# Kernel optimization log

Hardware: AMD Instinct MI355X
Metric: run time of the kernel (lower is better)

## Reference

```python
import jax, jax.numpy as jnp
import numpy as np

B, T, I, H, L, O = 2048, 512, 1, 64, 2, 1


def _lstm_layer(x, Wih, Whh, b):
    """Single LSTM layer, batch_first x: [B, T, in] -> [B, T, H].
    PyTorch gate order: i, f, g, o. b = b_ih + b_hh (folded)."""
    Bn = x.shape[0]
    Hn = Whh.shape[1]
    # Precompute input contribution for all timesteps (hoisted out of scan)
    xg = jnp.einsum('bti,gi->btg', x, Wih) + b  # [B, T, 4H]

    def step(carry, xg_t):
        h, c = carry
        g = xg_t + h @ Whh.T  # [B, 4H]
        i, f, gg, o = jnp.split(g, 4, axis=-1)
        i = jax.nn.sigmoid(i)
        f = jax.nn.sigmoid(f)
        gg = jnp.tanh(gg)
        o = jax.nn.sigmoid(o)
        c = f * c + i * gg
        h = o * jnp.tanh(c)
        return (h, c), h

    h0 = jnp.zeros((Bn, Hn), x.dtype)
    c0 = jnp.zeros((Bn, Hn), x.dtype)
    (_, _), hs = jax.lax.scan(step, (h0, c0), jnp.swapaxes(xg, 0, 1))  # hs: [T, B, H]
    return jnp.swapaxes(hs, 0, 1)


def setup_inputs() -> dict:
    key = jax.random.key(0)
    ks = jax.random.split(key, 11)
    s = 1.0 / np.sqrt(H)  # torch default uniform bound
    u = lambda k, shp: jax.random.uniform(k, shp, jnp.float32, -s, s)
    return {
        'x': jax.random.normal(ks[0], (B, T, I), jnp.float32),
        'Wih0': u(ks[1], (4 * H, I)),
        'Whh0': u(ks[2], (4 * H, H)),
        'bih0': u(ks[3], (4 * H,)),
        'bhh0': u(ks[4], (4 * H,)),
        'Wih1': u(ks[5], (4 * H, H)),
        'Whh1': u(ks[6], (4 * H, H)),
        'bih1': u(ks[7], (4 * H,)),
        'bhh1': u(ks[8], (4 * H,)),
        'fcW': u(ks[9], (O, H)),
        'fcb': u(ks[10], (O,)),
    }


def reference(x, Wih0, Whh0, bih0, bhh0, Wih1, Whh1, bih1, bhh1, fcW, fcb):
    h1 = _lstm_layer(x, Wih0, Whh0, bih0 + bhh0)   # [B, T, H]
    h2 = _lstm_layer(h1, Wih1, Whh1, bih1 + bhh1)  # [B, T, H]
    return h2[:, -1, :] @ fcW.T + fcb               # [B, O]
```

## Files before the change

### kernel.cpp

```cpp
#include <hip/hip_runtime.h>


#define TT 512
#define HH 64
#define BT 8

typedef __attribute__((ext_vector_type(8))) short short8;
typedef __attribute__((ext_vector_type(4))) float f32x4;

#define MFMA16 __builtin_amdgcn_mfma_f32_16x16x32_bf16

__device__ __forceinline__ float sigm(float x) {
    return __builtin_amdgcn_rcpf(1.f + __expf(-x));
}
__device__ __forceinline__ float tanh_f(float x) {
    return 1.f - 2.f * __builtin_amdgcn_rcpf(1.f + __expf(2.f * x));
}
__device__ __forceinline__ void cvt8(const float* p, short8& hi, short8& lo) {
    #pragma unroll
    for (int i = 0; i < 8; ++i) {
        float v = p[i];
        unsigned short h = (unsigned short)(__float_as_uint(v) >> 16);
        float r = v - __uint_as_float(((unsigned)h) << 16);
        unsigned short l = (unsigned short)(__float_as_uint(r) >> 16);
        hi[i] = (short)h;
        lo[i] = (short)l;
    }
}
__device__ __forceinline__ void split1(float v, unsigned short& h, unsigned short& l) {
    h = (unsigned short)(__float_as_uint(v) >> 16);
    float r = v - __uint_as_float(((unsigned)h) << 16);
    l = (unsigned short)(__float_as_uint(r) >> 16);
}
__device__ __forceinline__ float gate4(float pi, float pf, float pg, float po, float& c) {
    float gi = sigm(pi), gf = sigm(pf), gg = tanh_f(pg), go = sigm(po);
    c = fmaf(gf, c, gi * gg);
    return go * tanh_f(c);
}
__device__ __forceinline__ float dpp_ror8(float v) {
    return __int_as_float(__builtin_amdgcn_update_dpp(
        0, __float_as_int(v), 0x128, 0xF, 0xF, true));
}

__global__ __launch_bounds__(1024) void lstm_mfma(
    const float* __restrict__ x,
    const float* __restrict__ Wih0, const float* __restrict__ Whh0,
    const float* __restrict__ bih0, const float* __restrict__ bhh0,
    const float* __restrict__ Wih1, const float* __restrict__ Whh1,
    const float* __restrict__ bih1, const float* __restrict__ bhh1,
    const float* __restrict__ fcW, const float* __restrict__ fcb,
    float* __restrict__ out)
{
    __shared__ float xs[BT][TT + 1];
    __shared__ __align__(16) short aH1[2][2][2][64][8];
    __shared__ __align__(16) short aH2[2][2][2][64][8];
    __shared__ float hF[BT][HH + 1];
    __shared__ float fcw_s[HH];

    const int t    = threadIdx.x;
    const int lane = t & 63;
    const int w    = t >> 6;
    const bool isL1 = (w < 8);
    const int wv   = w & 7;
    const int b0   = blockIdx.x * BT;
    const int m    = lane & 15;
    const int q    = lane >> 4;

    for (int i = t; i < BT * TT; i += 1024)
        xs[i >> 9][i & (TT - 1)] = x[(size_t)(b0 + (i >> 9)) * TT + (i & (TT - 1))];
    {
        int* z1 = (int*)aH1;
        for (int i = t; i < 2048; i += 1024) z1[i] = 0;
        int* z2 = (int*)aH2;
        for (int i = t; i < 2048; i += 1024) z2[i] = 0;
    }
    if (t < HH) fcw_s[t] = fcW[t];

    short8 aWh[2][4], aWl[2][4];
    {
        const float* Ws01 = isL1 ? Whh0 : Wih1;
        #pragma unroll
        for (int i = 0; i < 2; ++i) {
            const int mtg = 2 * wv + i;
            const int rho = (m & 3) * 64 + 4 * mtg + (m >> 2);
            cvt8(Ws01 + rho * HH +      q * 8, aWh[i][0], aWl[i][0]);
            cvt8(Ws01 + rho * HH + 32 + q * 8, aWh[i][1], aWl[i][1]);
            if (!isL1) {
                cvt8(Whh1 + rho * HH +      q * 8, aWh[i][2], aWl[i][2]);
                cvt8(Whh1 + rho * HH + 32 + q * 8, aWh[i][3], aWl[i][3]);
            }
        }
    }

    const int ts  = (m >> 3) & 1;
    const int jpk = 8 * wv + 4 * ts + q;
    const int bpk = m & 7;
    float wxb[4], bia[4];
    #pragma unroll
    for (int v = 0; v < 4; ++v) {
        if (isL1) {
            wxb[v] = Wih0[v * 64 + jpk];
            bia[v] = bih0[v * 64 + jpk] + bhh0[v * 64 + jpk];
        } else {
            wxb[v] = 0.f;
            bia[v] = bih1[v * 64 + jpk] + bhh1[v * 64 + jpk];
        }
    }
    const int skt = jpk >> 5;
    const int ssl = bpk + 16 * ((jpk >> 3) & 3);
    const int sse = jpk & 7;
    float c = 0.f;

    __syncthreads();

    #pragma unroll 2
    for (int k = 0; k < TT; ++k) {
        const int p = k & 1, pn = p ^ 1;

        if (isL1) {
            short8 bh0 = *(const short8*)&aH1[p][0][0][lane][0];
            short8 bl0 = *(const short8*)&aH1[p][0][1][lane][0];
            short8 bh1 = *(const short8*)&aH1[p][1][0][lane][0];
            short8 bl1 = *(const short8*)&aH1[p][1][1][lane][0];
            f32x4 acc0 = {0.f, 0.f, 0.f, 0.f}, acc1 = acc0;
            acc0 = MFMA16(aWh[0][0], bh0, acc0, 0, 0, 0);
            acc0 = MFMA16(aWl[0][0], bh0, acc0, 0, 0, 0);
            acc0 = MFMA16(aWh[0][0], bl0, acc0, 0, 0, 0);
            acc0 = MFMA16(aWh[0][1], bh1, acc0, 0, 0, 0);
            acc0 = MFMA16(aWl[0][1], bh1, acc0, 0, 0, 0);
            acc0 = MFMA16(aWh[0][1], bl1, acc0, 0, 0, 0);
            acc1 = MFMA16(aWh[1][0], bh0, acc1, 0, 0, 0);
            acc1 = MFMA16(aWl[1][0], bh0, acc1, 0, 0, 0);
            acc1 = MFMA16(aWh[1][0], bl0, acc1, 0, 0, 0);
            acc1 = MFMA16(aWh[1][1], bh1, acc1, 0, 0, 0);
            acc1 = MFMA16(aWl[1][1], bh1, acc1, 0, 0, 0);
            acc1 = MFMA16(aWh[1][1], bl1, acc1, 0, 0, 0);
            f32x4 mv, pk;
            #pragma unroll
            for (int r = 0; r < 4; ++r) mv[r] = dpp_ror8(acc1[r]);
            #pragma unroll
            for (int r = 0; r < 4; ++r) pk[r] = (m < 8) ? acc0[r] : mv[r];
            float xb = xs[bpk][k];
            float h1 = gate4(pk[0] + fmaf(wxb[0], xb, bia[0]),
                             pk[1] + fmaf(wxb[1], xb, bia[1]),
                             pk[2] + fmaf(wxb[2], xb, bia[2]),
                             pk[3] + fmaf(wxb[3], xb, bia[3]), c);
            unsigned short hh, hl;
            split1(h1, hh, hl);
            aH1[pn][skt][0][ssl][sse] = (short)hh;
            aH1[pn][skt][1][ssl][sse] = (short)hl;
        } else if (k > 0) {
            short8 b1h0 = *(const short8*)&aH1[p][0][0][lane][0];
            short8 b1l0 = *(const short8*)&aH1[p][0][1][lane][0];
            short8 b1h1 = *(const short8*)&aH1[p][1][0][lane][0];
            short8 b1l1 = *(const short8*)&aH1[p][1][1][lane][0];
            short8 b2h0 = *(const short8*)&aH2[p][0][0][lane][0];
            short8 b2l0 = *(const short8*)&aH2[p][0][1][lane][0];
            short8 b2h1 = *(const short8*)&aH2[p][1][0][lane][0];
            short8 b2l1 = *(const short8*)&aH2[p][1][1][lane][0];
            f32x4 acc0 = {0.f, 0.f, 0.f, 0.f}, acc1 = acc0;
            acc0 = MFMA16(aWh[0][0], b1h0, acc0, 0, 0, 0);
            acc0 = MFMA16(aWl[0][0], b1h0, acc0, 0, 0, 0);
            acc0 = MFMA16(aWh[0][0], b1l0, acc0, 0, 0, 0);
            acc0 = MFMA16(aWh[0][1], b1h1, acc0, 0, 0, 0);
            acc0 = MFMA16(aWl[0][1], b1h1, acc0, 0, 0, 0);
            acc0 = MFMA16(aWh[0][1], b1l1, acc0, 0, 0, 0);
            acc0 = MFMA16(aWh[0][2], b2h0, acc0, 0, 0, 0);
            acc0 = MFMA16(aWl[0][2], b2h0, acc0, 0, 0, 0);
            acc0 = MFMA16(aWh[0][2], b2l0, acc0, 0, 0, 0);
            acc0 = MFMA16(aWh[0][3], b2h1, acc0, 0, 0, 0);
            acc0 = MFMA16(aWl[0][3], b2h1, acc0, 0, 0, 0);
            acc0 = MFMA16(aWh[0][3], b2l1, acc0, 0, 0, 0);
            acc1 = MFMA16(aWh[1][0], b1h0, acc1, 0, 0, 0);
            acc1 = MFMA16(aWl[1][0], b1h0, acc1, 0, 0, 0);
            acc1 = MFMA16(aWh[1][0], b1l0, acc1, 0, 0, 0);
            acc1 = MFMA16(aWh[1][1], b1h1, acc1, 0, 0, 0);
            acc1 = MFMA16(aWl[1][1], b1h1, acc1, 0, 0, 0);
            acc1 = MFMA16(aWh[1][1], b1l1, acc1, 0, 0, 0);
            acc1 = MFMA16(aWh[1][2], b2h0, acc1, 0, 0, 0);
            acc1 = MFMA16(aWl[1][2], b2h0, acc1, 0, 0, 0);
            acc1 = MFMA16(aWh[1][2], b2l0, acc1, 0, 0, 0);
            acc1 = MFMA16(aWh[1][3], b2h1, acc1, 0, 0, 0);
            acc1 = MFMA16(aWl[1][3], b2h1, acc1, 0, 0, 0);
            acc1 = MFMA16(aWh[1][3], b2l1, acc1, 0, 0, 0);
            f32x4 mv, pk;
            #pragma unroll
            for (int r = 0; r < 4; ++r) mv[r] = dpp_ror8(acc1[r]);
            #pragma unroll
            for (int r = 0; r < 4; ++r) pk[r] = (m < 8) ? acc0[r] : mv[r];
            float h2 = gate4(pk[0] + bia[0], pk[1] + bia[1],
                             pk[2] + bia[2], pk[3] + bia[3], c);
            unsigned short hh, hl;
            split1(h2, hh, hl);
            aH2[pn][skt][0][ssl][sse] = (short)hh;
            aH2[pn][skt][1][ssl][sse] = (short)hl;
        }
        __syncthreads();
    }

    if (!isL1) {
        short8 b1h0 = *(const short8*)&aH1[0][0][0][lane][0];
        short8 b1l0 = *(const short8*)&aH1[0][0][1][lane][0];
        short8 b1h1 = *(const short8*)&aH1[0][1][0][lane][0];
        short8 b1l1 = *(const short8*)&aH1[0][1][1][lane][0];
        short8 b2h0 = *(const short8*)&aH2[0][0][0][lane][0];
        short8 b2l0 = *(const short8*)&aH2[0][0][1][lane][0];
        short8 b2h1 = *(const short8*)&aH2[0][1][0][lane][0];
        short8 b2l1 = *(const short8*)&aH2[0][1][1][lane][0];
        f32x4 acc0 = {0.f, 0.f, 0.f, 0.f}, acc1 = acc0;
        acc0 = MFMA16(aWh[0][0], b1h0, acc0, 0, 0, 0);
        acc0 = MFMA16(aWl[0][0], b1h0, acc0, 0, 0, 0);
        acc0 = MFMA16(aWh[0][0], b1l0, acc0, 0, 0, 0);
        acc0 = MFMA16(aWh[0][1], b1h1, acc0, 0, 0, 0);
        acc0 = MFMA16(aWl[0][1], b1h1, acc0, 0, 0, 0);
        acc0 = MFMA16(aWh[0][1], b1l1, acc0, 0, 0, 0);
        acc0 = MFMA16(aWh[0][2], b2h0, acc0, 0, 0, 0);
        acc0 = MFMA16(aWl[0][2], b2h0, acc0, 0, 0, 0);
        acc0 = MFMA16(aWh[0][2], b2l0, acc0, 0, 0, 0);
        acc0 = MFMA16(aWh[0][3], b2h1, acc0, 0, 0, 0);
        acc0 = MFMA16(aWl[0][3], b2h1, acc0, 0, 0, 0);
        acc0 = MFMA16(aWh[0][3], b2l1, acc0, 0, 0, 0);
        acc1 = MFMA16(aWh[1][0], b1h0, acc1, 0, 0, 0);
        acc1 = MFMA16(aWl[1][0], b1h0, acc1, 0, 0, 0);
        acc1 = MFMA16(aWh[1][0], b1l0, acc1, 0, 0, 0);
        acc1 = MFMA16(aWh[1][1], b1h1, acc1, 0, 0, 0);
        acc1 = MFMA16(aWl[1][1], b1h1, acc1, 0, 0, 0);
        acc1 = MFMA16(aWh[1][1], b1l1, acc1, 0, 0, 0);
        acc1 = MFMA16(aWh[1][2], b2h0, acc1, 0, 0, 0);
        acc1 = MFMA16(aWl[1][2], b2h0, acc1, 0, 0, 0);
        acc1 = MFMA16(aWh[1][2], b2l0, acc1, 0, 0, 0);
        acc1 = MFMA16(aWh[1][3], b2h1, acc1, 0, 0, 0);
        acc1 = MFMA16(aWl[1][3], b2h1, acc1, 0, 0, 0);
        acc1 = MFMA16(aWh[1][3], b2l1, acc1, 0, 0, 0);
        f32x4 mv, pk;
        #pragma unroll
        for (int r = 0; r < 4; ++r) mv[r] = dpp_ror8(acc1[r]);
        #pragma unroll
        for (int r = 0; r < 4; ++r) pk[r] = (m < 8) ? acc0[r] : mv[r];
        float h2 = gate4(pk[0] + bia[0], pk[1] + bia[1],
                         pk[2] + bia[2], pk[3] + bia[3], c);
        hF[bpk][jpk] = h2;
    }
    __syncthreads();

    if (t < BT) {
        float s = fcb[0];
        #pragma unroll 8
        for (int j = 0; j < HH; ++j)
            s = fmaf(hF[t][j], fcw_s[j], s);
        out[b0 + t] = s;
    }
}

extern "C" void kernel_launch(void* const* d_in, const int* in_sizes, int n_in,
                              void* d_out, int out_size, void* d_ws, size_t ws_size,
                              hipStream_t stream) {
    const float* x    = (const float*)d_in[0];
    const float* Wih0 = (const float*)d_in[1];
    const float* Whh0 = (const float*)d_in[2];
    const float* bih0 = (const float*)d_in[3];
    const float* bhh0 = (const float*)d_in[4];
    const float* Wih1 = (const float*)d_in[5];
    const float* Whh1 = (const float*)d_in[6];
    const float* bih1 = (const float*)d_in[7];
    const float* bhh1 = (const float*)d_in[8];
    const float* fcW  = (const float*)d_in[9];
    const float* fcb  = (const float*)d_in[10];
    float* out = (float*)d_out;

    lstm_mfma<<<dim3(2048 / BT), dim3(1024), 0, stream>>>(
        x, Wih0, Whh0, bih0, bhh0, Wih1, Whh1, bih1, bhh1, fcW, fcb, out);
}
```

Measured before the change: 492.4 us.

## Replace split-bf16 MFMA with split-int8 fixed-point MFMA and unify layer waves

Switches the recurrent matmuls from three-term split-bf16 MFMA to a two-level int8 fixed-point split (hi/lo bytes) using the i32 16x16x64 int8 MFMA, scaling weights and hidden states to fixed-point. It also restructures the work split so every wave handles both layers: one lane half computes layer 1 and the other half layer 2. This cuts the MFMA count per step from 12/24 to 9 per wave and halves LDS traffic for h. In exchange it adds quantization error from dropping the lo*lo term and fixed-point rounding, plus conversion overhead per step.

```diff
diff --git a/kernel.cpp b/kernel.cpp
--- a/kernel.cpp
+++ b/kernel.cpp
@@ -5,32 +5,19 @@
 #define HH 64
 #define BT 8
 
-typedef __attribute__((ext_vector_type(8))) short short8;
-typedef __attribute__((ext_vector_type(4))) float f32x4;
+typedef __attribute__((ext_vector_type(4))) int i32x4;
 
-#define MFMA16 __builtin_amdgcn_mfma_f32_16x16x32_bf16
+#define MFMAI8 __builtin_amdgcn_mfma_i32_16x16x64_i8
+
+#define WSCALE 260096.0f
+#define HSCALE 32512.0f
+constexpr float C_MID = (float)(256.0 / (260096.0 * 32512.0));
 
 __device__ __forceinline__ float sigm(float x) {
     return __builtin_amdgcn_rcpf(1.f + __expf(-x));
 }
 __device__ __forceinline__ float tanh_f(float x) {
     return 1.f - 2.f * __builtin_amdgcn_rcpf(1.f + __expf(2.f * x));
-}
-__device__ __forceinline__ void cvt8(const float* p, short8& hi, short8& lo) {
-    #pragma unroll
-    for (int i = 0; i < 8; ++i) {
-        float v = p[i];
-        unsigned short h = (unsigned short)(__float_as_uint(v) >> 16);
-        float r = v - __uint_as_float(((unsigned)h) << 16);
-        unsigned short l = (unsigned short)(__float_as_uint(r) >> 16);
-        hi[i] = (short)h;
-        lo[i] = (short)l;
-    }
-}
-__device__ __forceinline__ void split1(float v, unsigned short& h, unsigned short& l) {
-    h = (unsigned short)(__float_as_uint(v) >> 16);
-    float r = v - __uint_as_float(((unsigned)h) << 16);
-    l = (unsigned short)(__float_as_uint(r) >> 16);
 }
 __device__ __forceinline__ float gate4(float pi, float pf, float pg, float po, float& c) {
     float gi = sigm(pi), gf = sigm(pf), gg = tanh_f(pg), go = sigm(po);
@@ -40,6 +27,21 @@
 __device__ __forceinline__ float dpp_ror8(float v) {
     return __int_as_float(__builtin_amdgcn_update_dpp(
         0, __float_as_int(v), 0x128, 0xF, 0xF, true));
+}
+__device__ __forceinline__ void cvtW16(const float* __restrict__ p, i32x4& hi, i32x4& lo) {
+    #pragma unroll
+    for (int r = 0; r < 4; ++r) {
+        int hw = 0, lw = 0;
+        #pragma unroll
+        for (int b = 0; b < 4; ++b) {
+            int wq = (int)rintf(p[r * 4 + b] * WSCALE);
+            int h8 = (wq + 128) >> 8;
+            int l8 = wq - (h8 << 8);
+            hw |= (h8 & 0xFF) << (8 * b);
+            lw |= (l8 & 0xFF) << (8 * b);
+        }
+        hi[r] = hw; lo[r] = lw;
+    }
 }
 
 __global__ __launch_bounds__(1024) void lstm_mfma(
@@ -52,63 +54,45 @@
     float* __restrict__ out)
 {
     __shared__ float xs[BT][TT + 1];
-    __shared__ __align__(16) short aH1[2][2][2][64][8];
-    __shared__ __align__(16) short aH2[2][2][2][64][8];
+    __shared__ __align__(16) signed char aH[2][2][2][64][16];
     __shared__ float hF[BT][HH + 1];
     __shared__ float fcw_s[HH];
 
     const int t    = threadIdx.x;
     const int lane = t & 63;
     const int w    = t >> 6;
-    const bool isL1 = (w < 8);
-    const int wv   = w & 7;
     const int b0   = blockIdx.x * BT;
     const int m    = lane & 15;
     const int q    = lane >> 4;
+    const int ts   = m >> 3;
+    const int bpk  = m & 7;
+    const int jpk  = 4 * w + q;
 
     for (int i = t; i < BT * TT; i += 1024)
         xs[i >> 9][i & (TT - 1)] = x[(size_t)(b0 + (i >> 9)) * TT + (i & (TT - 1))];
     {
-        int* z1 = (int*)aH1;
-        for (int i = t; i < 2048; i += 1024) z1[i] = 0;
-        int* z2 = (int*)aH2;
-        for (int i = t; i < 2048; i += 1024) z2[i] = 0;
+        int* z = (int*)aH;
+        for (int i = t; i < 2048; i += 1024) z[i] = 0;
     }
     if (t < HH) fcw_s[t] = fcW[t];
 
-    short8 aWh[2][4], aWl[2][4];
+    i32x4 A0h, A0l, I1h, I1l, H1h, H1l;
     {
-        const float* Ws01 = isL1 ? Whh0 : Wih1;
-        #pragma unroll
-        for (int i = 0; i < 2; ++i) {
-            const int mtg = 2 * wv + i;
-            const int rho = (m & 3) * 64 + 4 * mtg + (m >> 2);
-            cvt8(Ws01 + rho * HH +      q * 8, aWh[i][0], aWl[i][0]);
-            cvt8(Ws01 + rho * HH + 32 + q * 8, aWh[i][1], aWl[i][1]);
-            if (!isL1) {
-                cvt8(Whh1 + rho * HH +      q * 8, aWh[i][2], aWl[i][2]);
-                cvt8(Whh1 + rho * HH + 32 + q * 8, aWh[i][3], aWl[i][3]);
-            }
-        }
+        const int rho = (m & 3) * 64 + 4 * w + (m >> 2);
+        cvtW16(Whh0 + rho * HH + q * 16, A0h, A0l);
+        cvtW16(Wih1 + rho * HH + q * 16, I1h, I1l);
+        cvtW16(Whh1 + rho * HH + q * 16, H1h, H1l);
     }
 
-    const int ts  = (m >> 3) & 1;
-    const int jpk = 8 * wv + 4 * ts + q;
-    const int bpk = m & 7;
     float wxb[4], bia[4];
     #pragma unroll
     for (int v = 0; v < 4; ++v) {
-        if (isL1) {
-            wxb[v] = Wih0[v * 64 + jpk];
-            bia[v] = bih0[v * 64 + jpk] + bhh0[v * 64 + jpk];
-        } else {
-            wxb[v] = 0.f;
-            bia[v] = bih1[v * 64 + jpk] + bhh1[v * 64 + jpk];
-        }
+        const int r = v * 64 + jpk;
+        if (ts) { wxb[v] = 0.f;     bia[v] = bih1[r] + bhh1[r]; }
+        else    { wxb[v] = Wih0[r]; bia[v] = bih0[r] + bhh0[r]; }
     }
-    const int skt = jpk >> 5;
-    const int ssl = bpk + 16 * ((jpk >> 3) & 3);
-    const int sse = jpk & 7;
+    const int wl = ((jpk >> 4) << 4) + bpk;
+    const int wb = jpk & 15;
     float c = 0.f;
 
     __syncthreads();
@@ -116,130 +100,69 @@
     #pragma unroll 2
     for (int k = 0; k < TT; ++k) {
         const int p = k & 1, pn = p ^ 1;
+        i32x4 bh1 = *(const i32x4*)&aH[0][p][0][lane][0];
+        i32x4 bl1 = *(const i32x4*)&aH[0][p][1][lane][0];
+        i32x4 bh2 = *(const i32x4*)&aH[1][p][0][lane][0];
+        i32x4 bl2 = *(const i32x4*)&aH[1][p][1][lane][0];
+        i32x4 z4 = {0, 0, 0, 0};
+        i32x4 aHHr = z4, aMDr = z4, bHHr = z4, bMDr = z4;
+        aHHr = MFMAI8(A0h, bh1, aHHr, 0, 0, 0);
+        bHHr = MFMAI8(I1h, bh1, bHHr, 0, 0, 0);
+        aMDr = MFMAI8(A0h, bl1, aMDr, 0, 0, 0);
+        bMDr = MFMAI8(I1h, bl1, bMDr, 0, 0, 0);
+        aMDr = MFMAI8(A0l, bh1, aMDr, 0, 0, 0);
+        bMDr = MFMAI8(I1l, bh1, bMDr, 0, 0, 0);
+        bHHr = MFMAI8(H1h, bh2, bHHr, 0, 0, 0);
+        bMDr = MFMAI8(H1h, bl2, bMDr, 0, 0, 0);
+        bMDr = MFMAI8(H1l, bh2, bMDr, 0, 0, 0);
 
-        if (isL1) {
-            short8 bh0 = *(const short8*)&aH1[p][0][0][lane][0];
-            short8 bl0 = *(const short8*)&aH1[p][0][1][lane][0];
-            short8 bh1 = *(const short8*)&aH1[p][1][0][lane][0];
-            short8 bl1 = *(const short8*)&aH1[p][1][1][lane][0];
-            f32x4 acc0 = {0.f, 0.f, 0.f, 0.f}, acc1 = acc0;
-            acc0 = MFMA16(aWh[0][0], bh0, acc0, 0, 0, 0);
-            acc0 = MFMA16(aWl[0][0], bh0, acc0, 0, 0, 0);
-            acc0 = MFMA16(aWh[0][0], bl0, acc0, 0, 0, 0);
-            acc0 = MFMA16(aWh[0][1], bh1, acc0, 0, 0, 0);
-            acc0 = MFMA16(aWl[0][1], bh1, acc0, 0, 0, 0);
-            acc0 = MFMA16(aWh[0][1], bl1, acc0, 0, 0, 0);
-            acc1 = MFMA16(aWh[1][0], bh0, acc1, 0, 0, 0);
-            acc1 = MFMA16(aWl[1][0], bh0, acc1, 0, 0, 0);
-            acc1 = MFMA16(aWh[1][0], bl0, acc1, 0, 0, 0);
-            acc1 = MFMA16(aWh[1][1], bh1, acc1, 0, 0, 0);
-            acc1 = MFMA16(aWl[1][1], bh1, acc1, 0, 0, 0);
-            acc1 = MFMA16(aWh[1][1], bl1, acc1, 0, 0, 0);
-            f32x4 mv, pk;
-            #pragma unroll
-            for (int r = 0; r < 4; ++r) mv[r] = dpp_ror8(acc1[r]);
-            #pragma unroll
-            for (int r = 0; r < 4; ++r) pk[r] = (m < 8) ? acc0[r] : mv[r];
-            float xb = xs[bpk][k];
-            float h1 = gate4(pk[0] + fmaf(wxb[0], xb, bia[0]),
-                             pk[1] + fmaf(wxb[1], xb, bia[1]),
-                             pk[2] + fmaf(wxb[2], xb, bia[2]),
-                             pk[3] + fmaf(wxb[3], xb, bia[3]), c);
-            unsigned short hh, hl;
-            split1(h1, hh, hl);
-            aH1[pn][skt][0][ssl][sse] = (short)hh;
-            aH1[pn][skt][1][ssl][sse] = (short)hl;
-        } else if (k > 0) {
-            short8 b1h0 = *(const short8*)&aH1[p][0][0][lane][0];
-            short8 b1l0 = *(const short8*)&aH1[p][0][1][lane][0];
-            short8 b1h1 = *(const short8*)&aH1[p][1][0][lane][0];
-            short8 b1l1 = *(const short8*)&aH1[p][1][1][lane][0];
-            short8 b2h0 = *(const short8*)&aH2[p][0][0][lane][0];
-            short8 b2l0 = *(const short8*)&aH2[p][0][1][lane][0];
-            short8 b2h1 = *(const short8*)&aH2[p][1][0][lane][0];
-            short8 b2l1 = *(const short8*)&aH2[p][1][1][lane][0];
-            f32x4 acc0 = {0.f, 0.f, 0.f, 0.f}, acc1 = acc0;
-            acc0 = MFMA16(aWh[0][0], b1h0, acc0, 0, 0, 0);
-            acc0 = MFMA16(aWl[0][0], b1h0, acc0, 0, 0, 0);
-            acc0 = MFMA16(aWh[0][0], b1l0, acc0, 0, 0, 0);
-            acc0 = MFMA16(aWh[0][1], b1h1, acc0, 0, 0, 0);
-            acc0 = MFMA16(aWl[0][1], b1h1, acc0, 0, 0, 0);
-            acc0 = MFMA16(aWh[0][1], b1l1, acc0, 0, 0, 0);
-            acc0 = MFMA16(aWh[0][2], b2h0, acc0, 0, 0, 0);
-            acc0 = MFMA16(aWl[0][2], b2h0, acc0, 0, 0, 0);
-            acc0 = MFMA16(aWh[0][2], b2l0, acc0, 0, 0, 0);
-            acc0 = MFMA16(aWh[0][3], b2h1, acc0, 0, 0, 0);
-            acc0 = MFMA16(aWl[0][3], b2h1, acc0, 0, 0, 0);
-            acc0 = MFMA16(aWh[0][3], b2l1, acc0, 0, 0, 0);
-            acc1 = MFMA16(aWh[1][0], b1h0, acc1, 0, 0, 0);
-            acc1 = MFMA16(aWl[1][0], b1h0, acc1, 0, 0, 0);
-            acc1 = MFMA16(aWh[1][0], b1l0, acc1, 0, 0, 0);
-            acc1 = MFMA16(aWh[1][1], b1h1, acc1, 0, 0, 0);
-            acc1 = MFMA16(aWl[1][1], b1h1, acc1, 0, 0, 0);
-            acc1 = MFMA16(aWh[1][1], b1l1, acc1, 0, 0, 0);
-            acc1 = MFMA16(aWh[1][2], b2h0, acc1, 0, 0, 0);
-            acc1 = MFMA16(aWl[1][2], b2h0, acc1, 0, 0, 0);
-            acc1 = MFMA16(aWh[1][2], b2l0, acc1, 0, 0, 0);
-            acc1 = MFMA16(aWh[1][3], b2h1, acc1, 0, 0, 0);
-            acc1 = MFMA16(aWl[1][3], b2h1, acc1, 0, 0, 0);
-            acc1 = MFMA16(aWh[1][3], b2l1, acc1, 0, 0, 0);
-            f32x4 mv, pk;
-            #pragma unroll
-            for (int r = 0; r < 4; ++r) mv[r] = dpp_ror8(acc1[r]);
-            #pragma unroll
-            for (int r = 0; r < 4; ++r) pk[r] = (m < 8) ? acc0[r] : mv[r];
-            float h2 = gate4(pk[0] + bia[0], pk[1] + bia[1],
-                             pk[2] + bia[2], pk[3] + bia[3], c);
-            unsigned short hh, hl;
-            split1(h2, hh, hl);
-            aH2[pn][skt][0][ssl][sse] = (short)hh;
-            aH2[pn][skt][1][ssl][sse] = (short)hl;
+        float pk4[4];
+        #pragma unroll
+        for (int r = 0; r < 4; ++r) {
+            float pa = (float)((aHHr[r] << 8) + aMDr[r]) * C_MID;
+            float pb = (float)((bHHr[r] << 8) + bMDr[r]) * C_MID;
+            float mv = dpp_ror8(pb);
+            pk4[r] = (m < 8) ? pa : mv;
         }
+        float xb = xs[bpk][k];
+        float hv = gate4(pk4[0] + fmaf(wxb[0], xb, bia[0]),
+                         pk4[1] + fmaf(wxb[1], xb, bia[1]),
+                         pk4[2] + fmaf(wxb[2], xb, bia[2]),
+                         pk4[3] + fmaf(wxb[3], xb, bia[3]), c);
+        if (k == 0) {
+            hv = ts ? 0.f : hv;
+            c  = ts ? 0.f : c;
+        }
+        int hq = __float_as_int(fmaf(hv, HSCALE, 12582912.f)) - 0x4B400000;
+        int h8 = (hq + 128) >> 8;
+        int l8 = hq - (h8 << 8);
+        aH[ts][pn][0][wl][wb] = (signed char)h8;
+        aH[ts][pn][1][wl][wb] = (signed char)l8;
         __syncthreads();
     }
 
-    if (!isL1) {
-        short8 b1h0 = *(const short8*)&aH1[0][0][0][lane][0];
-        short8 b1l0 = *(const short8*)&aH1[0][0][1][lane][0];
-        short8 b1h1 = *(const short8*)&aH1[0][1][0][lane][0];
-        short8 b1l1 = *(const short8*)&aH1[0][1][1][lane][0];
-        short8 b2h0 = *(const short8*)&aH2[0][0][0][lane][0];
-        short8 b2l0 = *(const short8*)&aH2[0][0][1][lane][0];
-        short8 b2h1 = *(const short8*)&aH2[0][1][0][lane][0];
-        short8 b2l1 = *(const short8*)&aH2[0][1][1][lane][0];
-        f32x4 acc0 = {0.f, 0.f, 0.f, 0.f}, acc1 = acc0;
-        acc0 = MFMA16(aWh[0][0], b1h0, acc0, 0, 0, 0);
-        acc0 = MFMA16(aWl[0][0], b1h0, acc0, 0, 0, 0);
-        acc0 = MFMA16(aWh[0][0], b1l0, acc0, 0, 0, 0);
-        acc0 = MFMA16(aWh[0][1], b1h1, acc0, 0, 0, 0);
-        acc0 = MFMA16(aWl[0][1], b1h1, acc0, 0, 0, 0);
-        acc0 = MFMA16(aWh[0][1], b1l1, acc0, 0, 0, 0);
-        acc0 = MFMA16(aWh[0][2], b2h0, acc0, 0, 0, 0);
-        acc0 = MFMA16(aWl[0][2], b2h0, acc0, 0, 0, 0);
-        acc0 = MFMA16(aWh[0][2], b2l0, acc0, 0, 0, 0);
-        acc0 = MFMA16(aWh[0][3], b2h1, acc0, 0, 0, 0);
-        acc0 = MFMA16(aWl[0][3], b2h1, acc0, 0, 0, 0);
-        acc0 = MFMA16(aWh[0][3], b2l1, acc0, 0, 0, 0);
-        acc1 = MFMA16(aWh[1][0], b1h0, acc1, 0, 0, 0);
-        acc1 = MFMA16(aWl[1][0], b1h0, acc1, 0, 0, 0);
-        acc1 = MFMA16(aWh[1][0], b1l0, acc1, 0, 0, 0);
-        acc1 = MFMA16(aWh[1][1], b1h1, acc1, 0, 0, 0);
-        acc1 = MFMA16(aWl[1][1], b1h1, acc1, 0, 0, 0);
-        acc1 = MFMA16(aWh[1][1], b1l1, acc1, 0, 0, 0);
-        acc1 = MFMA16(aWh[1][2], b2h0, acc1, 0, 0, 0);
-        acc1 = MFMA16(aWl[1][2], b2h0, acc1, 0, 0, 0);
-        acc1 = MFMA16(aWh[1][2], b2l0, acc1, 0, 0, 0);
-        acc1 = MFMA16(aWh[1][3], b2h1, acc1, 0, 0, 0);
-        acc1 = MFMA16(aWl[1][3], b2h1, acc1, 0, 0, 0);
-        acc1 = MFMA16(aWh[1][3], b2l1, acc1, 0, 0, 0);
-        f32x4 mv, pk;
+    {
+        i32x4 bh1 = *(const i32x4*)&aH[0][0][0][lane][0];
+        i32x4 bl1 = *(const i32x4*)&aH[0][0][1][lane][0];
+        i32x4 bh2 = *(const i32x4*)&aH[1][0][0][lane][0];
+        i32x4 bl2 = *(const i32x4*)&aH[1][0][1][lane][0];
+        i32x4 z4 = {0, 0, 0, 0};
+        i32x4 bHHr = z4, bMDr = z4;
+        bHHr = MFMAI8(I1h, bh1, bHHr, 0, 0, 0);
+        bMDr = MFMAI8(I1h, bl1, bMDr, 0, 0, 0);
+        bMDr = MFMAI8(I1l, bh1, bMDr, 0, 0, 0);
+        bHHr = MFMAI8(H1h, bh2, bHHr, 0, 0, 0);
+        bMDr = MFMAI8(H1h, bl2, bMDr, 0, 0, 0);
+        bMDr = MFMAI8(H1l, bh2, bMDr, 0, 0, 0);
+        float pk4[4];
         #pragma unroll
-        for (int r = 0; r < 4; ++r) mv[r] = dpp_ror8(acc1[r]);
-        #pragma unroll
-        for (int r = 0; r < 4; ++r) pk[r] = (m < 8) ? acc0[r] : mv[r];
-        float h2 = gate4(pk[0] + bia[0], pk[1] + bia[1],
-                         pk[2] + bia[2], pk[3] + bia[3], c);
-        hF[bpk][jpk] = h2;
+        for (int r = 0; r < 4; ++r) {
+            float pb = (float)((bHHr[r] << 8) + bMDr[r]) * C_MID;
+            pk4[r] = dpp_ror8(pb);
+        }
+        float hv = gate4(pk4[0] + bia[0], pk4[1] + bia[1],
+                         pk4[2] + bia[2], pk4[3] + bia[3], c);
+        if (ts) hF[bpk][jpk] = hv;
     }
     __syncthreads();
 
```

Result: faster. 445.8 us (-9.5%).
